# Kernel optimization log

Hardware: AMD Instinct MI355X
Metric: run time of the kernel (lower is better)

## Reference

```python
import jax, jax.numpy as jnp
import numpy as np
import math

B, S, H = 8, 1024, 2048
NQ, NKV, D = 32, 8, 64
MAX_SEQ = 1024

def _rope_tables(seq_len, dim):
    inv_freq = 1.0 / (10000.0 ** (jnp.arange(0, dim, 2, dtype=jnp.float32) / dim))
    t = jnp.arange(seq_len, dtype=jnp.float32)[:, None]
    freqs = t * inv_freq[None, :]            # [S, D/2]
    freqs = jnp.concatenate([freqs, freqs], axis=-1)  # [S, D]
    return jnp.cos(freqs), jnp.sin(freqs)

def _rotate_half(x):
    x1, x2 = jnp.split(x, 2, axis=-1)
    return jnp.concatenate([-x2, x1], axis=-1)

def setup_inputs() -> dict:
    key = jax.random.key(0)
    ks = jax.random.split(key, 5)
    sc = 1.0 / math.sqrt(H)
    return {
        "hidden_states": jax.random.normal(ks[0], (B, S, H), dtype=jnp.float32),
        "Wq": jax.random.normal(ks[1], (H, NQ * D), dtype=jnp.float32) * sc,
        "Wk": jax.random.normal(ks[2], (H, NKV * D), dtype=jnp.float32) * sc,
        "Wv": jax.random.normal(ks[3], (H, NKV * D), dtype=jnp.float32) * sc,
        "Wo": jax.random.normal(ks[4], (NQ * D, H), dtype=jnp.float32) * sc,
    }

def reference(hidden_states, Wq, Wk, Wv, Wo):
    b, s, _ = hidden_states.shape
    q = (hidden_states @ Wq).reshape(b, s, NQ, D)   # [b,s,32,64]
    k = (hidden_states @ Wk).reshape(b, s, NKV, D)  # [b,s,8,64]
    v = (hidden_states @ Wv).reshape(b, s, NKV, D)
    cos, sin = _rope_tables(s, D)                   # [s,D]
    cos = cos[None, :, None, :]                     # [1,s,1,D]
    sin = sin[None, :, None, :]
    q = q * cos + _rotate_half(q) * sin
    k = k * cos + _rotate_half(k) * sin
    # repeat_kv (GQA): [b,s,8,D] -> [b,s,32,D]
    n_rep = NQ // NKV
    k = jnp.repeat(k, n_rep, axis=2)
    v = jnp.repeat(v, n_rep, axis=2)
    scores = jnp.einsum("bqhd,bkhd->bhqk", q, k) / math.sqrt(D)
    causal = jnp.tril(jnp.ones((s, s), dtype=bool))
    scores = jnp.where(causal[None, None], scores, -jnp.inf)
    attn = jax.nn.softmax(scores, axis=-1)
    out = jnp.einsum("bhqk,bkhd->bqhd", attn, v).reshape(b, s, NQ * D)
    return out @ Wo
```

## Files before the change

kernel.cpp:

```cpp
#include <hip/hip_runtime.h>
#include <math.h>

#define BB 8
#define SS 1024
#define HH 2048
#define NQH 32
#define NKVH 8
#define DD 64
#define MROWS (BB*SS)

typedef __attribute__((ext_vector_type(8))) short bf16x8;
typedef __attribute__((ext_vector_type(4))) float f32x4;

__device__ __forceinline__ unsigned short f2bf(float x) {
    unsigned int u = __float_as_uint(x);
    unsigned int r = (u + 0x7FFFu + ((u >> 16) & 1u)) >> 16;
    return (unsigned short)r;
}
__device__ __forceinline__ float bf2f(unsigned short u) {
    return __uint_as_float(((unsigned int)u) << 16);
}

__device__ __forceinline__ void gload_lds16(const void* gsrc, void* ldst) {
    __builtin_amdgcn_global_load_lds(
        (const __attribute__((address_space(1))) unsigned int*)gsrc,
        (__attribute__((address_space(3))) unsigned int*)ldst,
        16, 0, 0);
}

__global__ void conv_bf16(const float* __restrict__ src,
                          unsigned short* __restrict__ dst, int n8)
{
    int i = blockIdx.x * 256 + threadIdx.x;
    if (i >= n8) return;
    const float4* s4 = (const float4*)src;
    float4 a = s4[i * 2], b = s4[i * 2 + 1];
    bf16x8 o;
    o[0] = (short)f2bf(a.x); o[1] = (short)f2bf(a.y);
    o[2] = (short)f2bf(a.z); o[3] = (short)f2bf(a.w);
    o[4] = (short)f2bf(b.x); o[5] = (short)f2bf(b.y);
    o[6] = (short)f2bf(b.z); o[7] = (short)f2bf(b.w);
    *(bf16x8*)(dst + (size_t)i * 8) = o;
}

__global__ __launch_bounds__(256) void transpose_conv(
    const float* __restrict__ W, unsigned short* __restrict__ WT, int K, int N)
{
    __shared__ unsigned short t[64][68];
    const int bn = blockIdx.x * 64;
    const int bk = blockIdx.y * 64;
    #pragma unroll
    for (int it = 0; it < 4; ++it) {
        int idx = it * 256 + threadIdx.x;
        int r  = idx >> 4;
        int cq = (idx & 15) * 4;
        float4 v = *(const float4*)(W + (size_t)(bk + r) * N + bn + cq);
        t[cq + 0][r] = f2bf(v.x);
        t[cq + 1][r] = f2bf(v.y);
        t[cq + 2][r] = f2bf(v.z);
        t[cq + 3][r] = f2bf(v.w);
    }
    __syncthreads();
    #pragma unroll
    for (int it = 0; it < 4; ++it) {
        int idx = it * 256 + threadIdx.x;
        int r  = idx >> 4;
        int cq = (idx & 15) * 4;
        ushort4 o;
        o.x = t[r][cq + 0]; o.y = t[r][cq + 1];
        o.z = t[r][cq + 2]; o.w = t[r][cq + 3];
        *(ushort4*)(WT + (size_t)(bn + r) * K + bk + cq) = o;
    }
}

template <typename OutT>
__global__ __launch_bounds__(256) void gemm_bf16(
    const unsigned short* __restrict__ A,
    const unsigned short* __restrict__ Bt,
    OutT* __restrict__ C, int M, int N, int K)
{
    __shared__ __align__(16) unsigned short As[128 * 32];
    __shared__ __align__(16) unsigned short Bs[128 * 32];
    const int tid = threadIdx.x;
    const int lane = tid & 63;
    const int w = tid >> 6;
    const int wr = w >> 1, wc = w & 1;
    const int l15 = lane & 15, lg = lane >> 4;
    const int bm = blockIdx.y * 128, bn = blockIdx.x * 128;

    f32x4 acc[4][4] = {};

    for (int k0 = 0; k0 < K; k0 += 32) {
        #pragma unroll
        for (int t = 0; t < 2; ++t) {
            int lin = t * 256 + tid;
            int row = lin >> 2, cg = lin & 3;
            gload_lds16(A  + (size_t)(bm + row) * K + k0 + cg * 8, As + (size_t)lin * 8);
            gload_lds16(Bt + (size_t)(bn + row) * K + k0 + cg * 8, Bs + (size_t)lin * 8);
        }
        __syncthreads();
        bf16x8 af[4], bfr[4];
        #pragma unroll
        for (int m = 0; m < 4; ++m)
            af[m] = *(const bf16x8*)(As + (wr * 64 + m * 16 + l15) * 32 + lg * 8);
        #pragma unroll
        for (int n = 0; n < 4; ++n)
            bfr[n] = *(const bf16x8*)(Bs + (wc * 64 + n * 16 + l15) * 32 + lg * 8);
        #pragma unroll
        for (int m = 0; m < 4; ++m)
            #pragma unroll
            for (int n = 0; n < 4; ++n)
                acc[m][n] = __builtin_amdgcn_mfma_f32_16x16x32_bf16(
                    af[m], bfr[n], acc[m][n], 0, 0, 0);
        __syncthreads();
    }

    #pragma unroll
    for (int m = 0; m < 4; ++m) {
        int row0 = bm + wr * 64 + m * 16 + lg * 4;
        #pragma unroll
        for (int n = 0; n < 4; ++n) {
            int col = bn + wc * 64 + n * 16 + l15;
            #pragma unroll
            for (int r = 0; r < 4; ++r) {
                float v = acc[m][n][r];
                if constexpr (sizeof(OutT) == 2)
                    C[(size_t)(row0 + r) * N + col] = (OutT)f2bf(v);
                else
                    C[(size_t)(row0 + r) * N + col] = v;
            }
        }
    }
}

__global__ void rope_bf16(unsigned short* __restrict__ Q,
                          unsigned short* __restrict__ KV)
{
    int idx = blockIdx.x * 256 + threadIdx.x;
    const int totQ = MROWS * NQH * 32;
    unsigned short* x;
    int j, pos;
    if (idx < totQ) {
        j = idx & 31;
        int hd = idx >> 5;
        x = Q + (size_t)hd * 64;
        pos = (hd >> 5) & (SS - 1);
    } else {
        idx -= totQ;
        j = idx & 31;
        int hd = idx >> 5;
        int row = hd >> 3, head = hd & 7;
        x = KV + (size_t)row * 1024 + head * 64;
        pos = row & (SS - 1);
    }
    float ang = (float)pos * __expf(-(float)j * 0.28782314f);
    float s, c;
    __sincosf(ang, &s, &c);
    float x1 = bf2f(x[j]), x2 = bf2f(x[j + 32]);
    x[j]      = f2bf(x1 * c - x2 * s);
    x[j + 32] = f2bf(x2 * c + x1 * s);
}

#define VST 88

__global__ __launch_bounds__(256) void attn_bf16(
    unsigned short* Q,
    const unsigned short* KV)
{
    const int qt = (int)gridDim.x - 1 - (int)blockIdx.x;
    const int h = blockIdx.y, b = blockIdx.z;
    const int hk = h >> 2;
    const int tid = threadIdx.x;
    const int w = tid >> 6, lane = tid & 63;
    const int l15 = lane & 15, lg = lane >> 4;

    __shared__ __align__(16) unsigned short VT[2][64 * VST];
    __shared__ __align__(16) unsigned short Pl[4][32 * VST];

    const int wq0 = qt * 128 + w * 32;

    bf16x8 qf[2][2];
    #pragma unroll
    for (int n = 0; n < 2; ++n)
        #pragma unroll
        for (int kk = 0; kk < 2; ++kk)
            qf[n][kk] = *(const bf16x8*)(
                Q + (size_t)(b * SS + wq0 + n * 16 + l15) * 2048 + h * 64 + kk * 32 + lg * 8);

    f32x4 acc[2][4] = {};
    float m_run[2], l_run[2];
    #pragma unroll
    for (int n = 0; n < 2; ++n) { m_run[n] = -INFINITY; l_run[n] = 0.f; }

    const int nkt = 2 * qt + 2;

    {
        const unsigned short* vrow =
            KV + (size_t)(b * SS + lane) * 1024 + 512 + hk * 64 + w * 16;
        bf16x8 v0 = *(const bf16x8*)vrow;
        bf16x8 v1 = *(const bf16x8*)(vrow + 8);
        #pragma unroll
        for (int i = 0; i < 8; ++i) {
            VT[0][(w * 16 + i) * VST + lane]     = (unsigned short)v0[i];
            VT[0][(w * 16 + 8 + i) * VST + lane] = (unsigned short)v1[i];
        }
    }
    __syncthreads();

    for (int kt = 0; kt < nkt; ++kt) {
        const int cur = kt & 1;
        const bool pf = (kt + 1 < nkt);
        bf16x8 vp0, vp1;
        if (pf) {
            const unsigned short* vrow =
                KV + (size_t)(b * SS + (kt + 1) * 64 + lane) * 1024 + 512 + hk * 64 + w * 16;
            vp0 = *(const bf16x8*)vrow;
            vp1 = *(const bf16x8*)(vrow + 8);
        }

        const unsigned short* kbase = KV + (size_t)(b * SS + kt * 64) * 1024 + hk * 64;
        f32x4 sa[4][2] = {};
        #pragma unroll
        for (int m = 0; m < 4; ++m) {
            #pragma unroll
            for (int kk = 0; kk < 2; ++kk) {
                bf16x8 kf = *(const bf16x8*)(
                    kbase + (size_t)(m * 16 + l15) * 1024 + kk * 32 + lg * 8);
                sa[m][0] = __builtin_amdgcn_mfma_f32_16x16x32_bf16(kf, qf[0][kk], sa[m][0], 0, 0, 0);
                sa[m][1] = __builtin_amdgcn_mfma_f32_16x16x32_bf16(kf, qf[1][kk], sa[m][1], 0, 0, 0);
            }
        }

        float corr[2];
        #pragma unroll
        for (int n = 0; n < 2; ++n) {
            const int qg = wq0 + n * 16 + l15;
            float sv[4][4];
            float mx = -INFINITY;
            #pragma unroll
            for (int m = 0; m < 4; ++m)
                #pragma unroll
                for (int r = 0; r < 4; ++r) {
                    int keyg = kt * 64 + m * 16 + lg * 4 + r;
                    float v = sa[m][n][r] * 0.125f;
                    v = (keyg > qg) ? -INFINITY : v;
                    sv[m][r] = v;
                    mx = fmaxf(mx, v);
                }
            mx = fmaxf(mx, __shfl_xor(mx, 16));
            mx = fmaxf(mx, __shfl_xor(mx, 32));
            float mnew = fmaxf(m_run[n], mx);
            corr[n] = __expf(m_run[n] - mnew);
            float ps = 0.f;
            #pragma unroll
            for (int m = 0; m < 4; ++m)
                #pragma unroll
                for (int r = 0; r < 4; ++r) {
                    float p = __expf(sv[m][r] - mnew);
                    ps += p;
                    Pl[w][(n * 16 + l15) * VST + kt * 0 + m * 16 + lg * 4 + r] = f2bf(p);
                }
            ps += __shfl_xor(ps, 16);
            ps += __shfl_xor(ps, 32);
            l_run[n] = l_run[n] * corr[n] + ps;
            m_run[n] = mnew;
        }

        #pragma unroll
        for (int mq = 0; mq < 2; ++mq)
            #pragma unroll
            for (int r = 0; r < 4; ++r) {
                float cb = __shfl(corr[mq], lg * 4 + r);
                #pragma unroll
                for (int n = 0; n < 4; ++n) acc[mq][n][r] *= cb;
            }

        #pragma unroll
        for (int kk = 0; kk < 2; ++kk) {
            bf16x8 pa0 = *(const bf16x8*)(&Pl[w][(l15) * VST + kk * 32 + lg * 8]);
            bf16x8 pa1 = *(const bf16x8*)(&Pl[w][(16 + l15) * VST + kk * 32 + lg * 8]);
            #pragma unroll
            for (int n = 0; n < 4; ++n) {
                bf16x8 vb = *(const bf16x8*)(&VT[cur][(n * 16 + l15) * VST + kk * 32 + lg * 8]);
                acc[0][n] = __builtin_amdgcn_mfma_f32_16x16x32_bf16(pa0, vb, acc[0][n], 0, 0, 0);
                acc[1][n] = __builtin_amdgcn_mfma_f32_16x16x32_bf16(pa1, vb, acc[1][n], 0, 0, 0);
            }
        }

        if (pf) {
            #pragma unroll
            for (int i = 0; i < 8; ++i) {
                VT[cur ^ 1][(w * 16 + i) * VST + lane]     = (unsigned short)vp0[i];
                VT[cur ^ 1][(w * 16 + 8 + i) * VST + lane] = (unsigned short)vp1[i];
            }
        }
        __syncthreads();
    }

    float invl[2];
    #pragma unroll
    for (int n = 0; n < 2; ++n) invl[n] = 1.f / l_run[n];
    #pragma unroll
    for (int mq = 0; mq < 2; ++mq)
        #pragma unroll
        for (int r = 0; r < 4; ++r) {
            float ib = __shfl(invl[mq], lg * 4 + r);
            int qrow = wq0 + mq * 16 + lg * 4 + r;
            unsigned short* orow = Q + (size_t)(b * SS + qrow) * 2048 + h * 64;
            #pragma unroll
            for (int n = 0; n < 4; ++n)
                orow[n * 16 + l15] = f2bf(acc[mq][n][r] * ib);
        }
}

extern "C" void kernel_launch(void* const* d_in, const int* in_sizes, int n_in,
                              void* d_out, int out_size, void* d_ws, size_t ws_size,
                              hipStream_t stream)
{
    const float* X  = (const float*)d_in[0];
    const float* Wq = (const float*)d_in[1];
    const float* Wk = (const float*)d_in[2];
    const float* Wv = (const float*)d_in[3];
    const float* Wo = (const float*)d_in[4];
    float* out = (float*)d_out;

    char* ws = (char*)d_ws;
    unsigned short* Xbf  = (unsigned short*)(ws);
    unsigned short* WqT  = (unsigned short*)(ws + 33554432);
    unsigned short* WkvT = (unsigned short*)(ws + 41943040);
    unsigned short* Qbf  = (unsigned short*)(ws + 46137344);
    unsigned short* KVbf = (unsigned short*)(ws + 79691776);

    dim3 blk(256);

    conv_bf16<<<(MROWS * HH / 8 + 255) / 256, blk, 0, stream>>>(X, Xbf, MROWS * HH / 8);
    transpose_conv<<<dim3(HH / 64, HH / 64), blk, 0, stream>>>(Wq, WqT, HH, NQH * DD);
    transpose_conv<<<dim3((NKVH * DD) / 64, HH / 64), blk, 0, stream>>>(Wk, WkvT, HH, NKVH * DD);
    transpose_conv<<<dim3((NKVH * DD) / 64, HH / 64), blk, 0, stream>>>(Wv, WkvT + (size_t)(NKVH * DD) * HH, HH, NKVH * DD);

    gemm_bf16<unsigned short><<<dim3((NQH * DD) / 128, MROWS / 128), blk, 0, stream>>>(
        Xbf, WqT, Qbf, MROWS, NQH * DD, HH);
    gemm_bf16<unsigned short><<<dim3(1024 / 128, MROWS / 128), blk, 0, stream>>>(
        Xbf, WkvT, KVbf, MROWS, 1024, HH);

    rope_bf16<<<(MROWS * NQH * 32 + MROWS * NKVH * 32) / 256, blk, 0, stream>>>(Qbf, KVbf);

    attn_bf16<<<dim3(SS / 128, NQH, BB), blk, 0, stream>>>(Qbf, KVbf);

    transpose_conv<<<dim3(HH / 64, HH / 64), blk, 0, stream>>>(Wo, WqT, NQH * DD, HH);
    gemm_bf16<float><<<dim3(HH / 128, MROWS / 128), blk, 0, stream>>>(
        Qbf, WqT, out, MROWS, HH, NQH * DD);
}
```

Baseline: 660.5 us.

## Fuse QKV projection GEMM and rewrite attention with 32x32 MFMA register-resident P

```diff
diff --git a/kernel.cpp b/kernel.cpp
--- a/kernel.cpp
+++ b/kernel.cpp
@@ -8,9 +8,12 @@
 #define NKVH 8
 #define DD 64
 #define MROWS (BB*SS)
+#define QKVN 3072
 
 typedef __attribute__((ext_vector_type(8))) short bf16x8;
 typedef __attribute__((ext_vector_type(4))) float f32x4;
+typedef __attribute__((ext_vector_type(16))) float f32x16;
+typedef __attribute__((ext_vector_type(4))) unsigned int u32x4;
 
 __device__ __forceinline__ unsigned short f2bf(float x) {
     unsigned int u = __float_as_uint(x);
@@ -75,9 +78,9 @@
 
 template <typename OutT>
 __global__ __launch_bounds__(256) void gemm_bf16(
-    const unsigned short* __restrict__ A,
-    const unsigned short* __restrict__ Bt,
-    OutT* __restrict__ C, int M, int N, int K)
+    const unsigned short* __restrict__ A,  int lda,
+    const unsigned short* __restrict__ Bt, int ldb,
+    OutT* __restrict__ C, int ldc, int K)
 {
     __shared__ __align__(16) unsigned short As[128 * 32];
     __shared__ __align__(16) unsigned short Bs[128 * 32];
@@ -95,8 +98,8 @@
         for (int t = 0; t < 2; ++t) {
             int lin = t * 256 + tid;
             int row = lin >> 2, cg = lin & 3;
-            gload_lds16(A  + (size_t)(bm + row) * K + k0 + cg * 8, As + (size_t)lin * 8);
-            gload_lds16(Bt + (size_t)(bn + row) * K + k0 + cg * 8, Bs + (size_t)lin * 8);
+            gload_lds16(A  + (size_t)(bm + row) * lda + k0 + cg * 8, As + (size_t)lin * 8);
+            gload_lds16(Bt + (size_t)(bn + row) * ldb + k0 + cg * 8, Bs + (size_t)lin * 8);
         }
         __syncthreads();
         bf16x8 af[4], bfr[4];
@@ -125,16 +128,15 @@
             for (int r = 0; r < 4; ++r) {
                 float v = acc[m][n][r];
                 if constexpr (sizeof(OutT) == 2)
-                    C[(size_t)(row0 + r) * N + col] = (OutT)f2bf(v);
+                    C[(size_t)(row0 + r) * ldc + col] = (OutT)f2bf(v);
                 else
-                    C[(size_t)(row0 + r) * N + col] = v;
-            }
-        }
-    }
-}
-
-__global__ void rope_bf16(unsigned short* __restrict__ Q,
-                          unsigned short* __restrict__ KV)
+                    C[(size_t)(row0 + r) * ldc + col] = v;
+            }
+        }
+    }
+}
+
+__global__ void rope_bf16(unsigned short* __restrict__ QKV)
 {
     int idx = blockIdx.x * 256 + threadIdx.x;
     const int totQ = MROWS * NQH * 32;
@@ -143,14 +145,15 @@
     if (idx < totQ) {
         j = idx & 31;
         int hd = idx >> 5;
-        x = Q + (size_t)hd * 64;
-        pos = (hd >> 5) & (SS - 1);
+        int row = hd >> 5, head = hd & 31;
+        x = QKV + (size_t)row * QKVN + head * 64;
+        pos = row & (SS - 1);
     } else {
         idx -= totQ;
         j = idx & 31;
         int hd = idx >> 5;
         int row = hd >> 3, head = hd & 7;
-        x = KV + (size_t)row * 1024 + head * 64;
+        x = QKV + (size_t)row * QKVN + 2048 + head * 64;
         pos = row & (SS - 1);
     }
     float ang = (float)pos * __expf(-(float)j * 0.28782314f);
@@ -161,48 +164,43 @@
     x[j + 32] = f2bf(x2 * c + x1 * s);
 }
 
-#define VST 88
-
-__global__ __launch_bounds__(256) void attn_bf16(
-    unsigned short* Q,
-    const unsigned short* KV)
+__global__ __launch_bounds__(256) void attn_bf16(unsigned short* QKV)
 {
     const int qt = (int)gridDim.x - 1 - (int)blockIdx.x;
-    const int h = blockIdx.y, b = blockIdx.z;
-    const int hk = h >> 2;
+    const int hh = blockIdx.y, b = blockIdx.z;
+    const int hk = hh >> 2;
     const int tid = threadIdx.x;
     const int w = tid >> 6, lane = tid & 63;
-    const int l15 = lane & 15, lg = lane >> 4;
-
-    __shared__ __align__(16) unsigned short VT[2][64 * VST];
-    __shared__ __align__(16) unsigned short Pl[4][32 * VST];
+    const int l31 = lane & 31, h32 = lane >> 5;
+
+    __shared__ __align__(16) unsigned short VT[2][64 * 72];
 
     const int wq0 = qt * 128 + w * 32;
-
-    bf16x8 qf[2][2];
-    #pragma unroll
-    for (int n = 0; n < 2; ++n)
-        #pragma unroll
-        for (int kk = 0; kk < 2; ++kk)
-            qf[n][kk] = *(const bf16x8*)(
-                Q + (size_t)(b * SS + wq0 + n * 16 + l15) * 2048 + h * 64 + kk * 32 + lg * 8);
-
-    f32x4 acc[2][4] = {};
-    float m_run[2], l_run[2];
-    #pragma unroll
-    for (int n = 0; n < 2; ++n) { m_run[n] = -INFINITY; l_run[n] = 0.f; }
+    const int qg  = wq0 + l31;
+
+    bf16x8 qf[4];
+    {
+        const unsigned short* qrow =
+            QKV + (size_t)(b * SS + qg) * QKVN + hh * 64 + 8 * h32;
+        #pragma unroll
+        for (int kc = 0; kc < 4; ++kc)
+            qf[kc] = *(const bf16x8*)(qrow + kc * 16);
+    }
+
+    f32x16 acc_o[2] = {};
+    float m_run = -INFINITY, l_run = 0.f;
 
     const int nkt = 2 * qt + 2;
 
     {
         const unsigned short* vrow =
-            KV + (size_t)(b * SS + lane) * 1024 + 512 + hk * 64 + w * 16;
+            QKV + (size_t)(b * SS + lane) * QKVN + 2560 + hk * 64 + w * 16;
         bf16x8 v0 = *(const bf16x8*)vrow;
         bf16x8 v1 = *(const bf16x8*)(vrow + 8);
         #pragma unroll
         for (int i = 0; i < 8; ++i) {
-            VT[0][(w * 16 + i) * VST + lane]     = (unsigned short)v0[i];
-            VT[0][(w * 16 + 8 + i) * VST + lane] = (unsigned short)v1[i];
+            VT[0][(w * 16 + i) * 72 + lane]     = (unsigned short)v0[i];
+            VT[0][(w * 16 + 8 + i) * 72 + lane] = (unsigned short)v1[i];
         }
     }
     __syncthreads();
@@ -213,104 +211,116 @@
         bf16x8 vp0, vp1;
         if (pf) {
             const unsigned short* vrow =
-                KV + (size_t)(b * SS + (kt + 1) * 64 + lane) * 1024 + 512 + hk * 64 + w * 16;
+                QKV + (size_t)(b * SS + (kt + 1) * 64 + lane) * QKVN + 2560 + hk * 64 + w * 16;
             vp0 = *(const bf16x8*)vrow;
             vp1 = *(const bf16x8*)(vrow + 8);
         }
 
-        const unsigned short* kbase = KV + (size_t)(b * SS + kt * 64) * 1024 + hk * 64;
-        f32x4 sa[4][2] = {};
-        #pragma unroll
-        for (int m = 0; m < 4; ++m) {
-            #pragma unroll
-            for (int kk = 0; kk < 2; ++kk) {
-                bf16x8 kf = *(const bf16x8*)(
-                    kbase + (size_t)(m * 16 + l15) * 1024 + kk * 32 + lg * 8);
-                sa[m][0] = __builtin_amdgcn_mfma_f32_16x16x32_bf16(kf, qf[0][kk], sa[m][0], 0, 0, 0);
-                sa[m][1] = __builtin_amdgcn_mfma_f32_16x16x32_bf16(kf, qf[1][kk], sa[m][1], 0, 0, 0);
-            }
-        }
-
-        float corr[2];
-        #pragma unroll
-        for (int n = 0; n < 2; ++n) {
-            const int qg = wq0 + n * 16 + l15;
-            float sv[4][4];
-            float mx = -INFINITY;
-            #pragma unroll
-            for (int m = 0; m < 4; ++m)
+        f32x16 s[2] = {};
+        {
+            const unsigned short* kb =
+                QKV + (size_t)(b * SS + kt * 64) * QKVN + 2048 + hk * 64 + 8 * h32;
+            bf16x8 kf[2][4];
+            #pragma unroll
+            for (int kh = 0; kh < 2; ++kh)
                 #pragma unroll
-                for (int r = 0; r < 4; ++r) {
-                    int keyg = kt * 64 + m * 16 + lg * 4 + r;
-                    float v = sa[m][n][r] * 0.125f;
+                for (int kc = 0; kc < 4; ++kc)
+                    kf[kh][kc] = *(const bf16x8*)(kb + (size_t)(kh * 32 + l31) * QKVN + kc * 16);
+            #pragma unroll
+            for (int kh = 0; kh < 2; ++kh)
+                #pragma unroll
+                for (int kc = 0; kc < 4; ++kc)
+                    s[kh] = __builtin_amdgcn_mfma_f32_32x32x16_bf16(
+                        kf[kh][kc], qf[kc], s[kh], 0, 0, 0);
+        }
+
+        const bool full = (kt * 64 + 63 <= wq0);
+        float mx = -INFINITY;
+        #pragma unroll
+        for (int kh = 0; kh < 2; ++kh)
+            #pragma unroll
+            for (int r = 0; r < 16; ++r) {
+                float v = s[kh][r] * 0.125f;
+                if (!full) {
+                    int keyg = kt * 64 + kh * 32 + (r & 3) + 8 * (r >> 2) + 4 * h32;
                     v = (keyg > qg) ? -INFINITY : v;
-                    sv[m][r] = v;
-                    mx = fmaxf(mx, v);
                 }
-            mx = fmaxf(mx, __shfl_xor(mx, 16));
-            mx = fmaxf(mx, __shfl_xor(mx, 32));
-            float mnew = fmaxf(m_run[n], mx);
-            corr[n] = __expf(m_run[n] - mnew);
-            float ps = 0.f;
-            #pragma unroll
-            for (int m = 0; m < 4; ++m)
+                s[kh][r] = v;
+                mx = fmaxf(mx, v);
+            }
+        mx = fmaxf(mx, __shfl_xor(mx, 32));
+        const float mnew = fmaxf(m_run, mx);
+        const float corr = __expf(m_run - mnew);
+        float ps = 0.f;
+        #pragma unroll
+        for (int kh = 0; kh < 2; ++kh)
+            #pragma unroll
+            for (int r = 0; r < 16; ++r) {
+                float p = __expf(s[kh][r] - mnew);
+                s[kh][r] = p;
+                ps += p;
+            }
+        ps += __shfl_xor(ps, 32);
+        l_run = l_run * corr + ps;
+        m_run = mnew;
+        #pragma unroll
+        for (int d0 = 0; d0 < 2; ++d0)
+            #pragma unroll
+            for (int r = 0; r < 16; ++r)
+                acc_o[d0][r] *= corr;
+
+        #pragma unroll
+        for (int kh = 0; kh < 2; ++kh) {
+            #pragma unroll
+            for (int ks = 0; ks < 2; ++ks) {
+                unsigned int w0, w1, w2, w3;
+                asm("v_cvt_pk_bf16_f32 %0, %1, %2" : "=v"(w0) : "v"(s[kh][8*ks+0]), "v"(s[kh][8*ks+1]));
+                asm("v_cvt_pk_bf16_f32 %0, %1, %2" : "=v"(w2) : "v"(s[kh][8*ks+4]), "v"(s[kh][8*ks+5]));
+                asm("v_cvt_pk_bf16_f32 %0, %1, %2" : "=v"(w1) : "v"(s[kh][8*ks+2]), "v"(s[kh][8*ks+3]));
+                asm("v_cvt_pk_bf16_f32 %0, %1, %2" : "=v"(w3) : "v"(s[kh][8*ks+6]), "v"(s[kh][8*ks+7]));
+                asm("v_permlane32_swap_b32 %0, %1" : "+v"(w0), "+v"(w2));
+                asm("v_permlane32_swap_b32 %0, %1" : "+v"(w1), "+v"(w3));
+                union { u32x4 u; bf16x8 h; } pk;
+                pk.u = (u32x4){w0, w1, w2, w3};
                 #pragma unroll
-                for (int r = 0; r < 4; ++r) {
-                    float p = __expf(sv[m][r] - mnew);
-                    ps += p;
-                    Pl[w][(n * 16 + l15) * VST + kt * 0 + m * 16 + lg * 4 + r] = f2bf(p);
+                for (int d0 = 0; d0 < 2; ++d0) {
+                    bf16x8 vb = *(const bf16x8*)(
+                        &VT[cur][(d0 * 32 + l31) * 72 + kh * 32 + ks * 16 + 8 * h32]);
+                    acc_o[d0] = __builtin_amdgcn_mfma_f32_32x32x16_bf16(
+                        vb, pk.h, acc_o[d0], 0, 0, 0);
                 }
-            ps += __shfl_xor(ps, 16);
-            ps += __shfl_xor(ps, 32);
-            l_run[n] = l_run[n] * corr[n] + ps;
-            m_run[n] = mnew;
-        }
-
-        #pragma unroll
-        for (int mq = 0; mq < 2; ++mq)
-            #pragma unroll
-            for (int r = 0; r < 4; ++r) {
-                float cb = __shfl(corr[mq], lg * 4 + r);
-                #pragma unroll
-                for (int n = 0; n < 4; ++n) acc[mq][n][r] *= cb;
-            }
-
-        #pragma unroll
-        for (int kk = 0; kk < 2; ++kk) {
-            bf16x8 pa0 = *(const bf16x8*)(&Pl[w][(l15) * VST + kk * 32 + lg * 8]);
-            bf16x8 pa1 = *(const bf16x8*)(&Pl[w][(16 + l15) * VST + kk * 32 + lg * 8]);
-            #pragma unroll
-            for (int n = 0; n < 4; ++n) {
-                bf16x8 vb = *(const bf16x8*)(&VT[cur][(n * 16 + l15) * VST + kk * 32 + lg * 8]);
-                acc[0][n] = __builtin_amdgcn_mfma_f32_16x16x32_bf16(pa0, vb, acc[0][n], 0, 0, 0);
-                acc[1][n] = __builtin_amdgcn_mfma_f32_16x16x32_bf16(pa1, vb, acc[1][n], 0, 0, 0);
             }
         }
 
         if (pf) {
             #pragma unroll
             for (int i = 0; i < 8; ++i) {
-                VT[cur ^ 1][(w * 16 + i) * VST + lane]     = (unsigned short)vp0[i];
-                VT[cur ^ 1][(w * 16 + 8 + i) * VST + lane] = (unsigned short)vp1[i];
+                VT[cur ^ 1][(w * 16 + i) * 72 + lane]     = (unsigned short)vp0[i];
+                VT[cur ^ 1][(w * 16 + 8 + i) * 72 + lane] = (unsigned short)vp1[i];
             }
         }
         __syncthreads();
     }
 
-    float invl[2];
-    #pragma unroll
-    for (int n = 0; n < 2; ++n) invl[n] = 1.f / l_run[n];
-    #pragma unroll
-    for (int mq = 0; mq < 2; ++mq)
-        #pragma unroll
-        for (int r = 0; r < 4; ++r) {
-            float ib = __shfl(invl[mq], lg * 4 + r);
-            int qrow = wq0 + mq * 16 + lg * 4 + r;
-            unsigned short* orow = Q + (size_t)(b * SS + qrow) * 2048 + h * 64;
-            #pragma unroll
-            for (int n = 0; n < 4; ++n)
-                orow[n * 16 + l15] = f2bf(acc[mq][n][r] * ib);
-        }
+    {
+        unsigned short* ep = &VT[0][0] + w * (32 * 72);
+        const float inv = 1.f / l_run;
+        #pragma unroll
+        for (int d0 = 0; d0 < 2; ++d0)
+            #pragma unroll
+            for (int r = 0; r < 16; ++r) {
+                int d = d0 * 32 + (r & 3) + 8 * (r >> 2) + 4 * h32;
+                ep[l31 * 72 + d] = f2bf(acc_o[d0][r] * inv);
+            }
+        __syncthreads();
+        #pragma unroll
+        for (int u = 0; u < 4; ++u) {
+            int q = u * 8 + (lane >> 3);
+            int c = lane & 7;
+            *(bf16x8*)(QKV + (size_t)(b * SS + wq0 + q) * QKVN + hh * 64 + c * 8) =
+                *(const bf16x8*)(ep + q * 72 + c * 8);
+        }
+    }
 }
 
 extern "C" void kernel_launch(void* const* d_in, const int* in_sizes, int n_in,
@@ -325,29 +335,25 @@
     float* out = (float*)d_out;
 
     char* ws = (char*)d_ws;
-    unsigned short* Xbf  = (unsigned short*)(ws);
-    unsigned short* WqT  = (unsigned short*)(ws + 33554432);
-    unsigned short* WkvT = (unsigned short*)(ws + 41943040);
-    unsigned short* Qbf  = (unsigned short*)(ws + 46137344);
-    unsigned short* KVbf = (unsigned short*)(ws + 79691776);
+    unsigned short* Xbf    = (unsigned short*)(ws);
+    unsigned short* WqkvT  = (unsigned short*)(ws + 33554432);
+    unsigned short* QKV    = (unsigned short*)(ws + 46137344);
 
     dim3 blk(256);
 
     conv_bf16<<<(MROWS * HH / 8 + 255) / 256, blk, 0, stream>>>(X, Xbf, MROWS * HH / 8);
-    transpose_conv<<<dim3(HH / 64, HH / 64), blk, 0, stream>>>(Wq, WqT, HH, NQH * DD);
-    transpose_conv<<<dim3((NKVH * DD) / 64, HH / 64), blk, 0, stream>>>(Wk, WkvT, HH, NKVH * DD);
-    transpose_conv<<<dim3((NKVH * DD) / 64, HH / 64), blk, 0, stream>>>(Wv, WkvT + (size_t)(NKVH * DD) * HH, HH, NKVH * DD);
-
-    gemm_bf16<unsigned short><<<dim3((NQH * DD) / 128, MROWS / 128), blk, 0, stream>>>(
-        Xbf, WqT, Qbf, MROWS, NQH * DD, HH);
-    gemm_bf16<unsigned short><<<dim3(1024 / 128, MROWS / 128), blk, 0, stream>>>(
-        Xbf, WkvT, KVbf, MROWS, 1024, HH);
-
-    rope_bf16<<<(MROWS * NQH * 32 + MROWS * NKVH * 32) / 256, blk, 0, stream>>>(Qbf, KVbf);
-
-    attn_bf16<<<dim3(SS / 128, NQH, BB), blk, 0, stream>>>(Qbf, KVbf);
-
-    transpose_conv<<<dim3(HH / 64, HH / 64), blk, 0, stream>>>(Wo, WqT, NQH * DD, HH);
+    transpose_conv<<<dim3(2048 / 64, HH / 64), blk, 0, stream>>>(Wq, WqkvT, HH, 2048);
+    transpose_conv<<<dim3(512 / 64,  HH / 64), blk, 0, stream>>>(Wk, WqkvT + (size_t)2048 * HH, HH, 512);
+    transpose_conv<<<dim3(512 / 64,  HH / 64), blk, 0, stream>>>(Wv, WqkvT + (size_t)2560 * HH, HH, 512);
+
+    gemm_bf16<unsigned short><<<dim3(QKVN / 128, MROWS / 128), blk, 0, stream>>>(
+        Xbf, HH, WqkvT, HH, QKV, QKVN, HH);
+
+    rope_bf16<<<(MROWS * NQH * 32 + MROWS * NKVH * 32) / 256, blk, 0, stream>>>(QKV);
+
+    attn_bf16<<<dim3(SS / 128, NQH, BB), blk, 0, stream>>>(QKV);
+
+    transpose_conv<<<dim3(HH / 64, HH / 64), blk, 0, stream>>>(Wo, WqkvT, NQH * DD, HH);
     gemm_bf16<float><<<dim3(HH / 128, MROWS / 128), blk, 0, stream>>>(
-        Qbf, WqT, out, MROWS, HH, NQH * DD);
-}
+        QKV, QKVN, WqkvT, HH, out, HH, NQH * DD);
+}
```

Result: faster. 589.3 us (-10.8%).
